# Kernel optimization log

Measured on AMD Instinct MI355X. Metric: run time of the kernel, lower is better.

## Reference

```python
import jax, jax.numpy as jnp
import numpy as np


def setup_inputs() -> dict:
    key = jax.random.key(0)
    k1, k2, k3, k4 = jax.random.split(key, 4)
    B, H, W, C, NCLS = 128, 14, 14, 512, 200
    # post-ReLU-like non-negative feature map
    x = jax.random.uniform(k1, (B, H, W, C), dtype=jnp.float32)
    # one-hot-like logits for ground-truth labels (only argmax is used)
    gt = jax.random.normal(k2, (B, NCLS), dtype=jnp.float32)
    # positional template codebook; index [H, W] (== shape[0]-1) is the sentinel
    # 'negative' template used for all-zero channels
    t_p = jax.random.normal(k3, (H + 1, W + 1, H, W), dtype=jnp.float32)
    # per-class channel template, broadcast-multiplied with masked features
    class_templates = jax.random.uniform(k4, (NCLS, H, W, C), dtype=jnp.float32)
    return {"x": x, "gt": gt, "t_p": t_p, "class_templates": class_templates}


def reference(x, gt, t_p, class_templates):
    # x: [B, H, W, C] channels-last feature map
    B, H, W, C = x.shape
    flat = x.reshape(B, H * W, C)
    # global spatial argmax per (batch, channel) == max_pool_with_argmax over full extent
    idx = jnp.argmax(flat, axis=1)            # [B, C]
    h = idx // W                               # [B, C]
    w = idx % W                                # [B, C]
    # channels whose spatial max is exactly 0 get the sentinel template index
    empty = jnp.max(flat, axis=1) == 0.0       # [B, C]
    sentinel = t_p.shape[0] - 1
    h = jnp.where(empty, sentinel, h)
    w = jnp.where(empty, sentinel, w)
    # gather positional templates: [B, C, H, W] -> [B, H, W, C]
    templates = jnp.transpose(t_p[h, w], (0, 2, 3, 1))
    masked = jax.nn.relu(x * templates)
    # training branch with gt, reduce_loss=False: mask by the class template
    cls = jnp.argmax(gt, axis=1)               # [B]
    masked = masked * class_templates[cls]     # [B, H, W, C]
    return (masked, x, templates)
```

## Files before the change

### kernel.cpp

```cpp
#include <hip/hip_runtime.h>

#define B    128
#define H    14
#define W    14
#define C    512
#define NCLS 200
#define HW   (H * W)
#define TP_DIM 15
#define SENT_OFF ((14 * TP_DIM + 14) * HW)

__global__ void cls_argmax_kernel(const float* __restrict__ gt,
                                  int* __restrict__ cls) {
    int b = blockIdx.x * blockDim.x + threadIdx.x;
    if (b >= B) return;
    const float* g = gt + (size_t)b * NCLS;
    float best = g[0];
    int bi = 0;
    for (int i = 1; i < NCLS; ++i) {
        float v = g[i];
        if (v > best) { best = v; bi = i; }
    }
    cls[b] = bi;
}

__global__ void spatial_argmax_kernel(const float* __restrict__ x,
                                      int* __restrict__ hwoff) {
    int idx = blockIdx.x * blockDim.x + threadIdx.x;
    if (idx >= B * C) return;
    int b = idx / C;
    int c = idx - b * C;
    const float* xp = x + (size_t)b * HW * C + c;
    float best = xp[0];
    int bi = 0;
    for (int s = 1; s < HW; ++s) {
        float v = xp[(size_t)s * C];
        if (v > best) { best = v; bi = s; }
    }
    int off;
    if (best == 0.0f) {
        off = SENT_OFF;
    } else {
        int h = bi / W;
        int w = bi - h * W;
        off = (h * TP_DIM + w) * HW;
    }
    hwoff[idx] = off;
}

#define SPB 4

__global__ __launch_bounds__(C) void main_kernel(
        const float* __restrict__ x,
        const float* __restrict__ t_p,
        const float* __restrict__ ctpl,
        const int*   __restrict__ hwoff,
        const int*   __restrict__ cls,
        float*       __restrict__ out) {
    int blk = blockIdx.x;
    int b   = blk / (HW / SPB);
    int s0  = (blk - b * (HW / SPB)) * SPB;
    int c   = threadIdx.x;

    int off     = hwoff[b * C + c];
    int klass   = cls[b];

    const size_t plane = (size_t)B * HW * C;
    const size_t base  = ((size_t)b * HW + s0) * C + c;

    const float* __restrict__ trow = t_p + off;
    const float* __restrict__ xp   = x + base;
    const float* __restrict__ cp   = ctpl + ((size_t)klass * HW + s0) * C + c;
    float* __restrict__ out_m = out + base;
    float* __restrict__ out_x = out + plane + base;
    float* __restrict__ out_t = out + 2 * plane + base;

#pragma unroll
    for (int i = 0; i < SPB; ++i) {
        float t  = trow[s0 + i];
        float xv = xp[(size_t)i * C];
        float ct = cp[(size_t)i * C];
        float m  = fmaxf(xv * t, 0.0f) * ct;
        out_m[(size_t)i * C] = m;
        out_x[(size_t)i * C] = xv;
        out_t[(size_t)i * C] = t;
    }
}

extern "C" void kernel_launch(void* const* d_in, const int* in_sizes, int n_in,
                              void* d_out, int out_size, void* d_ws, size_t ws_size,
                              hipStream_t stream) {
    const float* x    = (const float*)d_in[0];
    const float* gt   = (const float*)d_in[1];
    const float* t_p  = (const float*)d_in[2];
    const float* ctpl = (const float*)d_in[3];
    float* out = (float*)d_out;

    int* hwoff = (int*)d_ws;
    int* cls   = hwoff + (size_t)B * C;

    hipLaunchKernelGGL(cls_argmax_kernel, dim3(1), dim3(128), 0, stream, gt, cls);

    hipLaunchKernelGGL(spatial_argmax_kernel,
                       dim3((B * C + 255) / 256), dim3(256), 0, stream,
                       x, hwoff);

    hipLaunchKernelGGL(main_kernel,
                       dim3(B * (HW / SPB)), dim3(C), 0, stream,
                       x, t_p, ctpl, hwoff, cls, out);
}
```

Baseline: 289.0 us.

## Merge argmax kernels and vectorize main kernel with float4 and nontemporal stores

The class argmax is folded into the spatial argmax kernel, which removes one launch. The main kernel now has each thread handle 4 channels with float4 loads of x and the class template. Each thread gathers 4 contiguous spatial template values per channel and transposes them in registers, and all three outputs are written with nontemporal float4 stores. This cuts the number of memory instructions and the scattered scalar template gathers, and should avoid polluting the cache with write-only data. In exchange, occupancy is lower because blocks are smaller with more work per thread.

Result: faster. 280.6 us (-2.9%).

```diff
diff --git a/kernel.cpp b/kernel.cpp
--- a/kernel.cpp
+++ b/kernel.cpp
@@ -9,29 +9,22 @@
 #define TP_DIM 15
 #define SENT_OFF ((14 * TP_DIM + 14) * HW)
 
-__global__ void cls_argmax_kernel(const float* __restrict__ gt,
-                                  int* __restrict__ cls) {
-    int b = blockIdx.x * blockDim.x + threadIdx.x;
-    if (b >= B) return;
-    const float* g = gt + (size_t)b * NCLS;
-    float best = g[0];
-    int bi = 0;
-    for (int i = 1; i < NCLS; ++i) {
-        float v = g[i];
-        if (v > best) { best = v; bi = i; }
-    }
-    cls[b] = bi;
-}
+typedef float  v4f __attribute__((ext_vector_type(4)));
+typedef int    v4i __attribute__((ext_vector_type(4)));
 
-__global__ void spatial_argmax_kernel(const float* __restrict__ x,
-                                      int* __restrict__ hwoff) {
-    int idx = blockIdx.x * blockDim.x + threadIdx.x;
-    if (idx >= B * C) return;
-    int b = idx / C;
-    int c = idx - b * C;
+__global__ __launch_bounds__(256) void argmax_kernel(
+        const float* __restrict__ x,
+        const float* __restrict__ gt,
+        int* __restrict__ hwoff,
+        int* __restrict__ cls) {
+    int idx = blockIdx.x * 256 + threadIdx.x;
+    int b = idx >> 9;
+    int c = idx & (C - 1);
+
     const float* xp = x + (size_t)b * HW * C + c;
     float best = xp[0];
     int bi = 0;
+#pragma unroll 14
     for (int s = 1; s < HW; ++s) {
         float v = xp[(size_t)s * C];
         if (v > best) { best = v; bi = s; }
@@ -45,11 +38,20 @@
         off = (h * TP_DIM + w) * HW;
     }
     hwoff[idx] = off;
+
+    if (idx < B) {
+        const float* g = gt + (size_t)idx * NCLS;
+        float gb = g[0];
+        int gi = 0;
+        for (int i = 1; i < NCLS; ++i) {
+            float v = g[i];
+            if (v > gb) { gb = v; gi = i; }
+        }
+        cls[idx] = gi;
+    }
 }
 
-#define SPB 4
-
-__global__ __launch_bounds__(C) void main_kernel(
+__global__ __launch_bounds__(128) void main_kernel(
         const float* __restrict__ x,
         const float* __restrict__ t_p,
         const float* __restrict__ ctpl,
@@ -57,32 +59,44 @@
         const int*   __restrict__ cls,
         float*       __restrict__ out) {
     int blk = blockIdx.x;
-    int b   = blk / (HW / SPB);
-    int s0  = (blk - b * (HW / SPB)) * SPB;
-    int c   = threadIdx.x;
+    int b   = blk / 49;
+    int s0  = (blk - b * 49) * 4;
+    int c0  = threadIdx.x * 4;
 
-    int off     = hwoff[b * C + c];
-    int klass   = cls[b];
+    v4i off = *(const v4i*)(hwoff + b * C + c0);
+    int klass = cls[b];
+
+    v4f t0 = *(const v4f*)(t_p + off.x + s0);
+    v4f t1 = *(const v4f*)(t_p + off.y + s0);
+    v4f t2 = *(const v4f*)(t_p + off.z + s0);
+    v4f t3 = *(const v4f*)(t_p + off.w + s0);
+    v4f tv[4];
+    tv[0] = (v4f){t0.x, t1.x, t2.x, t3.x};
+    tv[1] = (v4f){t0.y, t1.y, t2.y, t3.y};
+    tv[2] = (v4f){t0.z, t1.z, t2.z, t3.z};
+    tv[3] = (v4f){t0.w, t1.w, t2.w, t3.w};
 
     const size_t plane = (size_t)B * HW * C;
-    const size_t base  = ((size_t)b * HW + s0) * C + c;
-
-    const float* __restrict__ trow = t_p + off;
-    const float* __restrict__ xp   = x + base;
-    const float* __restrict__ cp   = ctpl + ((size_t)klass * HW + s0) * C + c;
+    const size_t base  = ((size_t)b * HW + s0) * C + c0;
+    const float* __restrict__ xp = x + base;
+    const float* __restrict__ cp = ctpl + ((size_t)klass * HW + s0) * C + c0;
     float* __restrict__ out_m = out + base;
     float* __restrict__ out_x = out + plane + base;
     float* __restrict__ out_t = out + 2 * plane + base;
 
 #pragma unroll
-    for (int i = 0; i < SPB; ++i) {
-        float t  = trow[s0 + i];
-        float xv = xp[(size_t)i * C];
-        float ct = cp[(size_t)i * C];
-        float m  = fmaxf(xv * t, 0.0f) * ct;
-        out_m[(size_t)i * C] = m;
-        out_x[(size_t)i * C] = xv;
-        out_t[(size_t)i * C] = t;
+    for (int i = 0; i < 4; ++i) {
+        v4f xv = *(const v4f*)(xp + (size_t)i * C);
+        v4f ct = *(const v4f*)(cp + (size_t)i * C);
+        v4f t  = tv[i];
+        v4f m;
+        m.x = fmaxf(xv.x * t.x, 0.0f) * ct.x;
+        m.y = fmaxf(xv.y * t.y, 0.0f) * ct.y;
+        m.z = fmaxf(xv.z * t.z, 0.0f) * ct.z;
+        m.w = fmaxf(xv.w * t.w, 0.0f) * ct.w;
+        __builtin_nontemporal_store(m,  (v4f*)(out_m + (size_t)i * C));
+        __builtin_nontemporal_store(xv, (v4f*)(out_x + (size_t)i * C));
+        __builtin_nontemporal_store(t,  (v4f*)(out_t + (size_t)i * C));
     }
 }
 
@@ -98,13 +112,11 @@
     int* hwoff = (int*)d_ws;
     int* cls   = hwoff + (size_t)B * C;
 
-    hipLaunchKernelGGL(cls_argmax_kernel, dim3(1), dim3(128), 0, stream, gt, cls);
-
-    hipLaunchKernelGGL(spatial_argmax_kernel,
-                       dim3((B * C + 255) / 256), dim3(256), 0, stream,
-                       x, hwoff);
+    hipLaunchKernelGGL(argmax_kernel,
+                       dim3((B * C) / 256), dim3(256), 0, stream,
+                       x, gt, hwoff, cls);
 
     hipLaunchKernelGGL(main_kernel,
-                       dim3(B * (HW / SPB)), dim3(C), 0, stream,
+                       dim3(B * (HW / 4)), dim3(128), 0, stream,
                        x, t_p, ctpl, hwoff, cls, out);
 }
```
